# Performance work log

Hardware: AMD Instinct MI355X
Metric: run time of the kernel (lower is better)

## Reference

```python
import jax, jax.numpy as jnp
import numpy as np

SCALE_FACTOR = 1.0  # init default; dropout_p=0 -> dropout is identity


def setup_inputs() -> dict:
    key = jax.random.key(0)
    kq, kk, kv = jax.random.split(key, 3)
    B, H, L, D = 4, 16, 2048, 128
    return {
        "query": jax.random.normal(kq, (B, H, L, D), dtype=jnp.float32),
        "key": jax.random.normal(kk, (B, H, L, D), dtype=jnp.float32),
        "value": jax.random.normal(kv, (B, H, L, D), dtype=jnp.float32),
    }


def reference(query, key, value):
    # qk = Q @ K^T, scaled by scale_factor (original divides by inverse scale)
    scores = jnp.einsum("bhqd,bhkd->bhqk", query, key) * SCALE_FACTOR
    probs = jax.nn.softmax(scores, axis=-1)  # dropout_p=0 -> identity
    return jnp.einsum("bhqk,bhkd->bhqd", probs, value)
```

## Files before the change

### kernel.cpp

```cpp
#include <hip/hip_runtime.h>
#include <hip/hip_bf16.h>
#include <stdint.h>

#define LL    2048
#define DD    128
#define KVB   32
#define NT    (LL / KVB)
#define WAVES 8
#define QW    32
#define QB    (QW * WAVES)

#define KROW     136
#define KPLANE_B (32 * KROW * 2)
#define VROW     36
#define VT_B     (DD * VROW * 4)
#define KHI_OFF  0
#define KLO_OFF  KPLANE_B
#define VT_OFF   (2 * KPLANE_B)
#define BUF_B    (VT_OFF + VT_B)
#define SMEM_B   (2 * BUF_B)

typedef __attribute__((ext_vector_type(4))) float          f32x4;
typedef __attribute__((ext_vector_type(8))) __bf16         bf16x8;
typedef __attribute__((ext_vector_type(8))) unsigned short u16x8;
typedef __attribute__((ext_vector_type(4))) unsigned int   u32x4;

static __device__ __forceinline__ unsigned bf16_rne(float x) {
  unsigned u = __builtin_bit_cast(unsigned, x);
  u += 0x7fffu + ((u >> 16) & 1u);
  return u >> 16;
}
static __device__ __forceinline__ unsigned pk_bf2(float x0, float x1) {
  return bf16_rne(x0) | (bf16_rne(x1) << 16);
}
static __device__ __forceinline__ void split_pk(float x0, float x1, unsigned& hi, unsigned& lo) {
  hi = pk_bf2(x0, x1);
  const float h0 = __builtin_bit_cast(float, hi << 16);
  const float h1 = __builtin_bit_cast(float, hi & 0xffff0000u);
  lo = pk_bf2(x0 - h0, x1 - h1);
}
static __device__ __forceinline__ f32x4 mfma16(u16x8 a, u16x8 b, f32x4 c) {
  return __builtin_amdgcn_mfma_f32_16x16x32_bf16(
      __builtin_bit_cast(bf16x8, a), __builtin_bit_cast(bf16x8, b), c, 0, 0, 0);
}

__global__ __launch_bounds__(512, 2) void fattn_kernel(
    const float* __restrict__ Qg, const float* __restrict__ Kg,
    const float* __restrict__ Vg, float* __restrict__ Og)
{
  extern __shared__ char smem[];

  const int bid  = (int)blockIdx.x;
  const int head = ((bid & 7) << 3) | (bid >> 6);
  const int qblk = (bid >> 3) & 7;
  const size_t hb = (size_t)head * (size_t)(LL * DD);
  const float* __restrict__ Qh = Qg + hb;
  const float* __restrict__ Kh = Kg + hb;
  const float* __restrict__ Vh = Vg + hb;
  float* __restrict__       Oh = Og + hb;

  const int tid  = (int)threadIdx.x;
  const int lane = tid & 63;
  const int wid  = tid >> 6;
  const int l15  = lane & 15;
  const int g    = lane >> 4;
  const int q0   = qblk * QB + wid * QW;

  u16x8 qhi[2][4], qlo[2][4];
#pragma unroll
  for (int qt = 0; qt < 2; ++qt) {
#pragma unroll
    for (int dc = 0; dc < 4; ++dc) {
      const float* p = Qh + (size_t)(q0 + qt * 16 + l15) * DD + dc * 32 + g * 8;
      const f32x4 a = *(const f32x4*)(p);
      const f32x4 b = *(const f32x4*)(p + 4);
      union { u16x8 v; unsigned u[4]; } H, L;
      split_pk(a[0], a[1], H.u[0], L.u[0]);
      split_pk(a[2], a[3], H.u[1], L.u[1]);
      split_pk(b[0], b[1], H.u[2], L.u[2]);
      split_pk(b[2], b[3], H.u[3], L.u[3]);
      qhi[qt][dc] = H.v; qlo[qt][dc] = L.v;
    }
  }

  const int kvr  = tid >> 4;
  const int d0   = (tid & 15) * 8;
  const int vswz = ((d0 >> 3) & 7) << 2;

  f32x4 kA, kB, vA, vB;

  {
    const float* kp = Kh + (size_t)kvr * DD + d0;
    const float* vp = Vh + (size_t)kvr * DD + d0;
    kA = *(const f32x4*)kp; kB = *(const f32x4*)(kp + 4);
    vA = *(const f32x4*)vp; vB = *(const f32x4*)(vp + 4);
  }

  auto stage = [&](int b) {
    unsigned short* kh = (unsigned short*)(smem + b * BUF_B + KHI_OFF);
    unsigned short* kl = (unsigned short*)(smem + b * BUF_B + KLO_OFF);
    unsigned*       vt = (unsigned*)(smem + b * BUF_B + VT_OFF);
    union { u16x8 v; unsigned u[4]; } H, L;
    split_pk(kA[0], kA[1], H.u[0], L.u[0]);
    split_pk(kA[2], kA[3], H.u[1], L.u[1]);
    split_pk(kB[0], kB[1], H.u[2], L.u[2]);
    split_pk(kB[2], kB[3], H.u[3], L.u[3]);
    *(u16x8*)(kh + kvr * KROW + d0) = H.v;
    *(u16x8*)(kl + kvr * KROW + d0) = L.v;
    const float vv[8] = {vA[0], vA[1], vA[2], vA[3], vB[0], vB[1], vB[2], vB[3]};
#pragma unroll
    for (int i = 0; i < 4; ++i) {
      unsigned h, l;
      split_pk(vv[2 * i], vv[2 * i + 1], h, l);
      const unsigned w0 = (h & 0xffffu) | (l << 16);
      const unsigned w1 = (h >> 16) | (l & 0xffff0000u);
      const int d = d0 + 2 * i;
      vt[(size_t)d * VROW + (kvr ^ vswz)]       = w0;
      vt[(size_t)(d + 1) * VROW + (kvr ^ vswz)] = w1;
    }
  };

  stage(0);
  __syncthreads();

  f32x4 oacc[8][2];
#pragma unroll
  for (int dt = 0; dt < 8; ++dt) {
    oacc[dt][0] = f32x4{0.f, 0.f, 0.f, 0.f};
    oacc[dt][1] = f32x4{0.f, 0.f, 0.f, 0.f};
  }
  float mrun[2] = {-INFINITY, -INFINITY};
  float lrun[2] = {0.f, 0.f};

  for (int t = 0; t < NT; ++t) {
    const int cb = t & 1;
    if (t + 1 < NT) {
      const float* kp = Kh + (size_t)((t + 1) * KVB + kvr) * DD + d0;
      const float* vp = Vh + (size_t)((t + 1) * KVB + kvr) * DD + d0;
      kA = *(const f32x4*)kp; kB = *(const f32x4*)(kp + 4);
      vA = *(const f32x4*)vp; vB = *(const f32x4*)(vp + 4);
    }

    const unsigned short* kh = (const unsigned short*)(smem + cb * BUF_B + KHI_OFF);
    const unsigned short* kl = (const unsigned short*)(smem + cb * BUF_B + KLO_OFF);
    f32x4 sacc[2][2];
    sacc[0][0] = f32x4{0.f,0.f,0.f,0.f}; sacc[0][1] = f32x4{0.f,0.f,0.f,0.f};
    sacc[1][0] = f32x4{0.f,0.f,0.f,0.f}; sacc[1][1] = f32x4{0.f,0.f,0.f,0.f};
#pragma unroll
    for (int dc = 0; dc < 4; ++dc) {
      u16x8 ah[2], al[2];
#pragma unroll
      for (int kvt = 0; kvt < 2; ++kvt) {
        const int off = (kvt * 16 + l15) * KROW + dc * 32 + g * 8;
        ah[kvt] = *(const u16x8*)(kh + off);
        al[kvt] = *(const u16x8*)(kl + off);
      }
#pragma unroll
      for (int kvt = 0; kvt < 2; ++kvt) {
#pragma unroll
        for (int qt = 0; qt < 2; ++qt) {
          sacc[kvt][qt] = mfma16(ah[kvt], qhi[qt][dc], sacc[kvt][qt]);
          sacc[kvt][qt] = mfma16(ah[kvt], qlo[qt][dc], sacc[kvt][qt]);
          sacc[kvt][qt] = mfma16(al[kvt], qhi[qt][dc], sacc[kvt][qt]);
        }
      }
    }

    u16x8 phi[2], plo[2];
#pragma unroll
    for (int qt = 0; qt < 2; ++qt) {
      float mx = sacc[0][qt][0];
      mx = fmaxf(mx, sacc[0][qt][1]); mx = fmaxf(mx, sacc[0][qt][2]); mx = fmaxf(mx, sacc[0][qt][3]);
      mx = fmaxf(mx, sacc[1][qt][0]); mx = fmaxf(mx, sacc[1][qt][1]);
      mx = fmaxf(mx, sacc[1][qt][2]); mx = fmaxf(mx, sacc[1][qt][3]);
      mx = fmaxf(mx, __shfl_xor(mx, 16));
      mx = fmaxf(mx, __shfl_xor(mx, 32));
      const float mnew  = fmaxf(mrun[qt], mx);
      const float alpha = __expf(mrun[qt] - mnew);
      mrun[qt] = mnew;
      float p[8];
      float rs = 0.f;
#pragma unroll
      for (int j = 0; j < 8; ++j) {
        const float e = __expf(sacc[j >> 2][qt][j & 3] - mnew);
        p[j] = e; rs += e;
      }
      rs += __shfl_xor(rs, 16);
      rs += __shfl_xor(rs, 32);
      lrun[qt] = lrun[qt] * alpha + rs;
#pragma unroll
      for (int dt = 0; dt < 8; ++dt) oacc[dt][qt] *= alpha;
      union { u16x8 v; unsigned u[4]; } PH, PL;
#pragma unroll
      for (int i = 0; i < 4; ++i) split_pk(p[2 * i], p[2 * i + 1], PH.u[i], PL.u[i]);
      phi[qt] = PH.v; plo[qt] = PL.v;
    }

    const unsigned* vt = (const unsigned*)(smem + cb * BUF_B + VT_OFF);
#pragma unroll
    for (int dt = 0; dt < 8; ++dt) {
      const int d  = dt * 16 + l15;
      const int sz = ((d >> 3) & 7) << 2;
      const unsigned* row = vt + (size_t)d * VROW;
      const u32x4 r0 = *(const u32x4*)(row + ((g * 4) ^ sz));
      const u32x4 r1 = *(const u32x4*)(row + ((16 + g * 4) ^ sz));
      union { u16x8 v; unsigned u[4]; } VH, VL;
      VH.u[0] = __builtin_amdgcn_perm(r0[1], r0[0], 0x05040100u);
      VH.u[1] = __builtin_amdgcn_perm(r0[3], r0[2], 0x05040100u);
      VH.u[2] = __builtin_amdgcn_perm(r1[1], r1[0], 0x05040100u);
      VH.u[3] = __builtin_amdgcn_perm(r1[3], r1[2], 0x05040100u);
      VL.u[0] = __builtin_amdgcn_perm(r0[1], r0[0], 0x07060302u);
      VL.u[1] = __builtin_amdgcn_perm(r0[3], r0[2], 0x07060302u);
      VL.u[2] = __builtin_amdgcn_perm(r1[1], r1[0], 0x07060302u);
      VL.u[3] = __builtin_amdgcn_perm(r1[3], r1[2], 0x07060302u);
#pragma unroll
      for (int qt = 0; qt < 2; ++qt) {
        oacc[dt][qt] = mfma16(VH.v, phi[qt], oacc[dt][qt]);
        oacc[dt][qt] = mfma16(VH.v, plo[qt], oacc[dt][qt]);
        oacc[dt][qt] = mfma16(VL.v, phi[qt], oacc[dt][qt]);
      }
    }

    if (t + 1 < NT) stage(cb ^ 1);
    __syncthreads();
  }

#pragma unroll
  for (int qt = 0; qt < 2; ++qt) {
    const float inv = 1.0f / lrun[qt];
    float* orow = Oh + (size_t)(q0 + qt * 16 + l15) * DD + g * 4;
#pragma unroll
    for (int dt = 0; dt < 8; ++dt) {
      f32x4 o = oacc[dt][qt];
      o *= inv;
      *(f32x4*)(orow + dt * 16) = o;
    }
  }
}

extern "C" void kernel_launch(void* const* d_in, const int* in_sizes, int n_in,
                              void* d_out, int out_size, void* d_ws, size_t ws_size,
                              hipStream_t stream)
{
  (void)in_sizes; (void)n_in; (void)out_size; (void)d_ws; (void)ws_size;
  const float* Q = (const float*)d_in[0];
  const float* K = (const float*)d_in[1];
  const float* V = (const float*)d_in[2];
  float* O = (float*)d_out;

  (void)hipFuncSetAttribute((const void*)fattn_kernel,
                            hipFuncAttributeMaxDynamicSharedMemorySize, SMEM_B);

  dim3 grid(64 * (LL / QB));
  dim3 block(WAVES * 64);
  fattn_kernel<<<grid, block, SMEM_B, stream>>>(Q, K, V, O);
}
```

Measured before the change: 597.0 us.

## Fold log2e into Q, defer softmax rescale, use hardware bf16 cvt and setprio

Q is pre-scaled by log2(e) so the softmax can use native exp2 instead of __expf. The running-max rescale of the output accumulators is skipped unless some row's max grows by more than a threshold (the FA4-style lazy rescale). Manual bf16 round-to-nearest-even is replaced with the compiler's __bf16 conversion, and the MFMA sections are wrapped in s_setprio to favour matrix issue across waves. Deferring the rescale lets exponentials reach up to 2^8 before renormalising, which slightly changes the numerics of the bf16 hi/lo split.

Measured after the change: 541.8 us. 9.2% less time.

```diff
diff --git a/kernel.cpp b/kernel.cpp
--- a/kernel.cpp
+++ b/kernel.cpp
@@ -20,24 +20,24 @@
 #define BUF_B    (VT_OFF + VT_B)
 #define SMEM_B   (2 * BUF_B)
 
+#define LOG2E 1.44269504088896340736f
+#define DEFER_THR 8.0f
+
 typedef __attribute__((ext_vector_type(4))) float          f32x4;
 typedef __attribute__((ext_vector_type(8))) __bf16         bf16x8;
 typedef __attribute__((ext_vector_type(8))) unsigned short u16x8;
 typedef __attribute__((ext_vector_type(4))) unsigned int   u32x4;
 
-static __device__ __forceinline__ unsigned bf16_rne(float x) {
-  unsigned u = __builtin_bit_cast(unsigned, x);
-  u += 0x7fffu + ((u >> 16) & 1u);
-  return u >> 16;
+static __device__ __forceinline__ unsigned short bf16b(float x) {
+  return __builtin_bit_cast(unsigned short, (__bf16)x);
 }
 static __device__ __forceinline__ unsigned pk_bf2(float x0, float x1) {
-  return bf16_rne(x0) | (bf16_rne(x1) << 16);
+  return (unsigned)bf16b(x0) | ((unsigned)bf16b(x1) << 16);
 }
 static __device__ __forceinline__ void split_pk(float x0, float x1, unsigned& hi, unsigned& lo) {
   hi = pk_bf2(x0, x1);
-  const float h0 = __builtin_bit_cast(float, hi << 16);
-  const float h1 = __builtin_bit_cast(float, hi & 0xffff0000u);
-  lo = pk_bf2(x0 - h0, x1 - h1);
+  lo = pk_bf2(x0 - __builtin_bit_cast(float, hi << 16),
+              x1 - __builtin_bit_cast(float, hi & 0xffff0000u));
 }
 static __device__ __forceinline__ f32x4 mfma16(u16x8 a, u16x8 b, f32x4 c) {
   return __builtin_amdgcn_mfma_f32_16x16x32_bf16(
@@ -72,8 +72,9 @@
 #pragma unroll
     for (int dc = 0; dc < 4; ++dc) {
       const float* p = Qh + (size_t)(q0 + qt * 16 + l15) * DD + dc * 32 + g * 8;
-      const f32x4 a = *(const f32x4*)(p);
-      const f32x4 b = *(const f32x4*)(p + 4);
+      f32x4 a = *(const f32x4*)(p);
+      f32x4 b = *(const f32x4*)(p + 4);
+      a *= LOG2E; b *= LOG2E;
       union { u16x8 v; unsigned u[4]; } H, L;
       split_pk(a[0], a[1], H.u[0], L.u[0]);
       split_pk(a[2], a[3], H.u[1], L.u[1]);
@@ -146,6 +147,7 @@
     f32x4 sacc[2][2];
     sacc[0][0] = f32x4{0.f,0.f,0.f,0.f}; sacc[0][1] = f32x4{0.f,0.f,0.f,0.f};
     sacc[1][0] = f32x4{0.f,0.f,0.f,0.f}; sacc[1][1] = f32x4{0.f,0.f,0.f,0.f};
+    __builtin_amdgcn_s_setprio(1);
 #pragma unroll
     for (int dc = 0; dc < 4; ++dc) {
       u16x8 ah[2], al[2];
@@ -165,6 +167,7 @@
         }
       }
     }
+    __builtin_amdgcn_s_setprio(0);
 
     u16x8 phi[2], plo[2];
 #pragma unroll
@@ -175,21 +178,25 @@
       mx = fmaxf(mx, sacc[1][qt][2]); mx = fmaxf(mx, sacc[1][qt][3]);
       mx = fmaxf(mx, __shfl_xor(mx, 16));
       mx = fmaxf(mx, __shfl_xor(mx, 32));
-      const float mnew  = fmaxf(mrun[qt], mx);
-      const float alpha = __expf(mrun[qt] - mnew);
-      mrun[qt] = mnew;
+      if (!__all(mx <= mrun[qt] + DEFER_THR)) {
+        const float mnew  = fmaxf(mrun[qt], mx);
+        const float alpha = __builtin_amdgcn_exp2f(mrun[qt] - mnew);
+        mrun[qt] = mnew;
+        lrun[qt] *= alpha;
+#pragma unroll
+        for (int dt = 0; dt < 8; ++dt) oacc[dt][qt] *= alpha;
+      }
+      const float mcur = mrun[qt];
       float p[8];
       float rs = 0.f;
 #pragma unroll
       for (int j = 0; j < 8; ++j) {
-        const float e = __expf(sacc[j >> 2][qt][j & 3] - mnew);
+        const float e = __builtin_amdgcn_exp2f(sacc[j >> 2][qt][j & 3] - mcur);
         p[j] = e; rs += e;
       }
       rs += __shfl_xor(rs, 16);
       rs += __shfl_xor(rs, 32);
-      lrun[qt] = lrun[qt] * alpha + rs;
-#pragma unroll
-      for (int dt = 0; dt < 8; ++dt) oacc[dt][qt] *= alpha;
+      lrun[qt] += rs;
       union { u16x8 v; unsigned u[4]; } PH, PL;
 #pragma unroll
       for (int i = 0; i < 4; ++i) split_pk(p[2 * i], p[2 * i + 1], PH.u[i], PL.u[i]);
@@ -197,6 +204,7 @@
     }
 
     const unsigned* vt = (const unsigned*)(smem + cb * BUF_B + VT_OFF);
+    __builtin_amdgcn_s_setprio(1);
 #pragma unroll
     for (int dt = 0; dt < 8; ++dt) {
       const int d  = dt * 16 + l15;
@@ -220,6 +228,7 @@
         oacc[dt][qt] = mfma16(VL.v, phi[qt], oacc[dt][qt]);
       }
     }
+    __builtin_amdgcn_s_setprio(0);
 
     if (t + 1 < NT) stage(cb ^ 1);
     __syncthreads();
```
